# Performance work log

Measured on AMD Instinct MI355X. Metric: run time of the kernel, lower is better.

The kernel has to match this reference:

```python
import jax, jax.numpy as jnp
import numpy as np

N_NODES = 50000


def gcn_layer(x, W, b, src, dst, norm):
    # x: [N, Fin] -> [N, Fout]; PyG GCNConv: x' = D^-1/2 (A+I) D^-1/2 (x W) + b
    h = x @ W
    msg = h[src] * norm[:, None]              # gather + scale per edge (incl. self loops)
    out = jax.ops.segment_sum(msg, dst, num_segments=N_NODES)
    return out + b


def setup_inputs() -> dict:
    key = jax.random.key(0)
    ks = jax.random.split(key, 12)
    F_in, F_hid, T, E = 128, 128, 10, 1600000
    features = jax.random.normal(ks[0], (N_NODES, F_in), dtype=jnp.float32)
    edges = jax.random.randint(ks[1], (2, E), 0, N_NODES, dtype=jnp.int64)
    s = 1.0 / np.sqrt(F_in)
    W0 = jax.random.uniform(ks[2], (F_in, F_hid), jnp.float32, -s, s)
    b0 = jnp.zeros((F_hid,), jnp.float32)
    W1 = jax.random.uniform(ks[3], (F_hid, F_hid), jnp.float32, -s, s)
    b1 = jnp.zeros((F_hid,), jnp.float32)
    W2 = jax.random.uniform(ks[4], (F_hid, F_hid), jnp.float32, -s, s)
    b2 = jnp.zeros((F_hid,), jnp.float32)
    Wout = jax.random.uniform(ks[5], (F_hid, T), jnp.float32, -s, s)
    bout = jax.random.uniform(ks[6], (T,), jnp.float32, -s, s)
    return {"features": features, "edges": edges, "W0": W0, "b0": b0,
            "W1": W1, "b1": b1, "W2": W2, "b2": b2, "Wout": Wout, "bout": bout}


def reference(features, edges, W0, b0, W1, b1, W2, b2, Wout, bout):
    # Add self loops once; edge structure shared across layers.
    loop = jnp.arange(N_NODES, dtype=edges.dtype)
    src = jnp.concatenate([edges[0], loop])
    dst = jnp.concatenate([edges[1], loop])
    deg = jax.ops.segment_sum(jnp.ones_like(dst, dtype=features.dtype), dst,
                              num_segments=N_NODES)
    dinv = jnp.where(deg > 0, jax.lax.rsqrt(deg), 0.0)
    norm = dinv[src] * dinv[dst]              # [E + N]

    x = gcn_layer(features, W0, b0, src, dst, norm)
    x = gcn_layer(x, W1, b1, src, dst, norm)
    x = gcn_layer(x, W2, b2, src, dst, norm)

    pooled = jnp.mean(x, axis=0)              # [F_hid]
    logits = pooled @ Wout + bout             # [T]
    return jax.nn.log_softmax(logits, axis=0).reshape(1, -1)
```

## Files before the change

kernel.cpp:

```cpp
#include <hip/hip_runtime.h>


#define FDIM 128
#define HSZ 12500
#define NBG 64
#define BSZ 98
#define NBKT 512
#define SCB 256
#define STG 6400


__global__ void __launch_bounds__(1024)
k1_count_deg(const int* __restrict__ edges, int E, int e4, int N,
             int* __restrict__ blockCnt, int* __restrict__ partial) {
  __shared__ int h[HSZ];
  __shared__ int cnt[NBKT];
  const int t = threadIdx.x;
  const int bid = blockIdx.x;
  const int g = bid >> 6, j = bid & (NBG - 1);
  const int lo = g * HSZ;
  const int hi = min(N, lo + HSZ);
  const int hs = hi - lo;
  for (int i = t; i < hs; i += 1024) h[i] = 0;
  if (t < NBKT) cnt[t] = 0;
  __syncthreads();

  const int per4 = (e4 + SCB - 1) / SCB;
  const int i0 = bid * per4;
  const int i1 = min(e4, i0 + per4);
  const int4* s4 = (const int4*)edges;
  for (int i = i0 + t; i < i1; i += 1024) {
    int4 s = s4[i];
    atomicAdd(&cnt[s.x / BSZ], 1);
    atomicAdd(&cnt[s.y / BSZ], 1);
    atomicAdd(&cnt[s.z / BSZ], 1);
    atomicAdd(&cnt[s.w / BSZ], 1);
  }
  if (bid == 0) {
    for (int e = 4 * e4 + t; e < E; e += 1024)
      atomicAdd(&cnt[edges[e] / BSZ], 1);
  }

  const int4* d4 = (const int4*)(edges + E);
  for (int i = j * 1024 + t; i < e4; i += NBG * 1024) {
    int4 d = d4[i];
    if (d.x >= lo && d.x < hi) atomicAdd(&h[d.x - lo], 1);
    if (d.y >= lo && d.y < hi) atomicAdd(&h[d.y - lo], 1);
    if (d.z >= lo && d.z < hi) atomicAdd(&h[d.z - lo], 1);
    if (d.w >= lo && d.w < hi) atomicAdd(&h[d.w - lo], 1);
  }
  if (j == 0) {
    const int* dst = edges + E;
    for (int e = 4 * e4 + t; e < E; e += 1024) {
      int d = dst[e];
      if (d >= lo && d < hi) atomicAdd(&h[d - lo], 1);
    }
  }
  __syncthreads();
  if (t < NBKT) blockCnt[bid * NBKT + t] = cnt[t];
  int* op = partial + (size_t)bid * HSZ;
  for (int i = t; i < hs; i += 1024) op[i] = h[i];
}


__global__ void __launch_bounds__(256)
k2_scatter_dinv(const int* __restrict__ edges, int E, int e4, int N,
                const int* __restrict__ blockCnt,
                const int* __restrict__ partial,
                int* __restrict__ bucket, int* __restrict__ meta,
                float* __restrict__ dinv) {
  const int bid = blockIdx.x;
  const int t = threadIdx.x;

  if (bid >= SCB) {
    int n = (bid - SCB) * 256 + t;
    if (n < N) {
      int gg = n / HSZ, off = n - gg * HSZ;
      const int* p = partial + ((size_t)gg * NBG) * HSZ + off;
      int s = 1;
      for (int jj = 0; jj < NBG; ++jj) s += p[(size_t)jj * HSZ];
      dinv[n] = rsqrtf((float)s);
    }
    return;
  }

  __shared__ int baseS[NBKT];
  __shared__ int off2[NBKT];
  __shared__ int offRun[NBKT];
  __shared__ int cntS[NBKT];
  __shared__ int wsum[4];
  __shared__ int stg[STG];

  const int lane = t & 63, wv = t >> 6;
  const int k0 = 2 * t, k1 = 2 * t + 1;
  const int c0 = blockCnt[bid * NBKT + k0];
  const int c1 = blockCnt[bid * NBKT + k1];
  int off0 = 0, off1 = 0, tot0 = 0, tot1 = 0;
  for (int b = 0; b < SCB; ++b) {
    int v0 = blockCnt[b * NBKT + k0];
    int v1 = blockCnt[b * NBKT + k1];
    if (b < bid) { off0 += v0; off1 += v1; }
    tot0 += v0; tot1 += v1;
  }
  int s = tot0 + tot1;
  int inc = s;
  #pragma unroll
  for (int o = 1; o < 64; o <<= 1) {
    int q = __shfl_up(inc, o, 64);
    if (lane >= o) inc += q;
  }
  if (lane == 63) wsum[wv] = inc;
  __syncthreads();
  int wb = 0;
  for (int w = 0; w < wv; ++w) wb += wsum[w];
  const int ex = wb + inc - s;
  baseS[k0] = ex + off0;
  baseS[k1] = ex + tot0 + off1;
  if (bid == 0) {
    meta[k0] = ex;            meta[k1] = ex + tot0;
    meta[NBKT + k0] = tot0;   meta[NBKT + k1] = tot1;
  }
  int s2 = c0 + c1;
  int inc2 = s2;
  #pragma unroll
  for (int o = 1; o < 64; o <<= 1) {
    int q = __shfl_up(inc2, o, 64);
    if (lane >= o) inc2 += q;
  }
  __syncthreads();
  if (lane == 63) wsum[wv] = inc2;
  __syncthreads();
  int wb2 = 0;
  for (int w = 0; w < wv; ++w) wb2 += wsum[w];
  const int ex2 = wb2 + inc2 - s2;
  off2[k0] = ex2;        off2[k1] = ex2 + c0;
  offRun[k0] = ex2;      offRun[k1] = ex2 + c0;
  cntS[k0] = c0;         cntS[k1] = c1;
  __syncthreads();

  const int per4 = (e4 + SCB - 1) / SCB;
  const int i0 = bid * per4;
  const int i1 = min(e4, i0 + per4);
  const int4* s4 = (const int4*)edges;
  const int4* d4 = (const int4*)(edges + E);
  for (int i = i0 + t; i < i1; i += 256) {
    int4 sv = s4[i];
    int4 dv = d4[i];
    int b, p;
    b = sv.x / BSZ; p = atomicAdd(&offRun[b], 1); stg[p] = ((sv.x - b * BSZ) << 16) | dv.x;
    b = sv.y / BSZ; p = atomicAdd(&offRun[b], 1); stg[p] = ((sv.y - b * BSZ) << 16) | dv.y;
    b = sv.z / BSZ; p = atomicAdd(&offRun[b], 1); stg[p] = ((sv.z - b * BSZ) << 16) | dv.z;
    b = sv.w / BSZ; p = atomicAdd(&offRun[b], 1); stg[p] = ((sv.w - b * BSZ) << 16) | dv.w;
  }
  if (bid == 0) {
    for (int e = 4 * e4 + t; e < E; e += 256) {
      int sv = edges[e], dv = edges[E + e];
      int b = sv / BSZ;
      int p = atomicAdd(&offRun[b], 1);
      stg[p] = ((sv - b * BSZ) << 16) | dv;
    }
  }
  __syncthreads();
  for (int k = t; k < NBKT; k += 256) {
    const int len = cntS[k];
    const int lb = off2[k];
    const int gb = baseS[k];
    for (int i = 0; i < len; ++i)
      bucket[gb + i] = stg[lb + i];
  }
}


__global__ void __launch_bounds__(1024)
pass_kernel(const int* __restrict__ bucket, const int* __restrict__ meta,
            const float* __restrict__ dinv, const float* __restrict__ win,
            float* __restrict__ wout, float* __restrict__ ssump,
            const float* __restrict__ feat, float* __restrict__ v0p,
            int N, int doV0) {
  __shared__ float uacc[16][100];
  __shared__ float ul[BSZ];
  __shared__ float red[16];
  __shared__ float partS[8][FDIM];
  const int t = threadIdx.x;
  const int wv = t >> 6;
  const int b = blockIdx.x;
  const int n0 = b * BSZ;
  const int ns = min(BSZ, N - n0);

  for (int i = t; i < 16 * 100; i += 1024)
    ((float*)uacc)[i] = 0.f;
  __syncthreads();

  const int base = meta[b];
  const int end = base + meta[NBKT + b];
  for (int i = base + t; i < end; i += 1024) {
    int p = bucket[i];
    atomicAdd(&uacc[wv][p >> 16], win[p & 0xFFFF]);
  }
  __syncthreads();

  float u = 0.f;
  if (t < ns) {
    float s = 0.f;
    #pragma unroll
    for (int k = 0; k < 16; ++k) s += uacc[k][t];
    int n = n0 + t;
    u = dinv[n] * (s + win[n]);
    if (wout) wout[n] = dinv[n] * u;
    ul[t] = u;
  } else if (t < BSZ) {
    ul[t] = 0.f;
  }
  if (ssump) {
    float a = u;
    for (int o = 32; o > 0; o >>= 1) a += __shfl_down(a, o, 64);
    if ((t & 63) == 0) red[wv] = a;
    __syncthreads();
    if (t == 0) {
      float s = 0.f;
      #pragma unroll
      for (int k = 0; k < 16; ++k) s += red[k];
      ssump[b] = s;
    }
  }
  if (doV0) {
    __syncthreads();
    const int f = t & (FDIM - 1);
    const int r8 = t >> 7;
    float acc = 0.f;
    for (int r = r8; r < ns; r += 8)
      acc += ul[r] * feat[(size_t)(n0 + r) * FDIM + f];
    partS[r8][f] = acc;
    __syncthreads();
    if (r8 == 0) {
      float s = 0.f;
      #pragma unroll
      for (int k = 0; k < 8; ++k) s += partS[k][f];
      v0p[(size_t)b * FDIM + f] = s;
    }
  }
}


__global__ void __launch_bounds__(1024)
final_kernel(const float* __restrict__ W0, const float* __restrict__ b0,
             const float* __restrict__ W1, const float* __restrict__ b1,
             const float* __restrict__ W2, const float* __restrict__ b2,
             const float* __restrict__ Wout, const float* __restrict__ bout,
             const float* __restrict__ v0p, int nv0,
             const float* __restrict__ ssumpA,
             const float* __restrict__ ssumpB,
             int nss,
             float* __restrict__ out, int N) {
  __shared__ float Wl[FDIM * FDIM];
  __shared__ float WoL[FDIM * 10];
  __shared__ float va[FDIM], vb[FDIM];
  __shared__ float part[8][FDIM];
  __shared__ float red0[16], red1[16];
  __shared__ float shS1, shS2;
  __shared__ float lg[10];
  const int t = threadIdx.x;
  const int f = t & (FDIM - 1);
  const int sl = t >> 7;

  {
    const float4* w4 = (const float4*)W0;
    float4* l4 = (float4*)Wl;
    #pragma unroll
    for (int i = 0; i < 4; ++i) l4[t + i * 1024] = w4[t + i * 1024];
    if (t < (FDIM * 10) / 4) ((float4*)WoL)[t] = ((const float4*)Wout)[t];
  }
  float acc = 0.f;
  for (int j = sl; j < nv0; j += 8) acc += v0p[(size_t)j * FDIM + f];
  part[sl][f] = acc;
  {
    float a0 = 0.f, a1 = 0.f;
    for (int j = t; j < nss; j += 1024) { a0 += ssumpA[j]; a1 += ssumpB[j]; }
    for (int o = 32; o > 0; o >>= 1) {
      a0 += __shfl_down(a0, o, 64);
      a1 += __shfl_down(a1, o, 64);
    }
    if ((t & 63) == 0) { red0[t >> 6] = a0; red1[t >> 6] = a1; }
  }
  __syncthreads();
  if (sl == 0) {
    float s = 0.f;
    #pragma unroll
    for (int j = 0; j < 8; ++j) s += part[j][f];
    va[f] = s;
  }
  if (t == 0) {
    float x = 0.f, y = 0.f;
    #pragma unroll
    for (int i = 0; i < 16; ++i) { x += red0[i]; y += red1[i]; }
    shS2 = x; shS1 = y;
  }
  __syncthreads();

  acc = 0.f;
  #pragma unroll
  for (int k = 0; k < 16; ++k) {
    int kk = sl * 16 + k;
    acc += va[kk] * Wl[kk * FDIM + f];
  }
  part[sl][f] = acc;
  __syncthreads();
  {
    const float4* w4 = (const float4*)W1;
    float4* l4 = (float4*)Wl;
    #pragma unroll
    for (int i = 0; i < 4; ++i) l4[t + i * 1024] = w4[t + i * 1024];
  }
  if (sl == 0) {
    float s = 0.f;
    #pragma unroll
    for (int j = 0; j < 8; ++j) s += part[j][f];
    vb[f] = s + shS1 * b0[f];
  }
  __syncthreads();

  acc = 0.f;
  #pragma unroll
  for (int k = 0; k < 16; ++k) {
    int kk = sl * 16 + k;
    acc += vb[kk] * Wl[kk * FDIM + f];
  }
  part[sl][f] = acc;
  __syncthreads();
  {
    const float4* w4 = (const float4*)W2;
    float4* l4 = (float4*)Wl;
    #pragma unroll
    for (int i = 0; i < 4; ++i) l4[t + i * 1024] = w4[t + i * 1024];
  }
  if (sl == 0) {
    float s = 0.f;
    #pragma unroll
    for (int j = 0; j < 8; ++j) s += part[j][f];
    va[f] = s + shS2 * b1[f];
  }
  __syncthreads();

  acc = 0.f;
  #pragma unroll
  for (int k = 0; k < 16; ++k) {
    int kk = sl * 16 + k;
    acc += va[kk] * Wl[kk * FDIM + f];
  }
  part[sl][f] = acc;
  __syncthreads();
  if (sl == 0) {
    float s = 0.f;
    #pragma unroll
    for (int j = 0; j < 8; ++j) s += part[j][f];
    vb[f] = s / (float)N + b2[f];
  }
  __syncthreads();

  if (t < 10) {
    float a = 0.f;
    for (int k = 0; k < FDIM; ++k) a += vb[k] * WoL[k * 10 + t];
    lg[t] = a + bout[t];
  }
  __syncthreads();
  if (t == 0) {
    float m = lg[0];
    for (int q = 1; q < 10; ++q) m = fmaxf(m, lg[q]);
    float s = 0.f;
    for (int q = 0; q < 10; ++q) s += expf(lg[q] - m);
    float lse = logf(s);
    for (int q = 0; q < 10; ++q) out[q] = lg[q] - m - lse;
  }
}


__global__ void __launch_bounds__(1024)
hist_deg_kernel(const int* __restrict__ edges, int E, int e4, int N,
                int* __restrict__ partial) {
  __shared__ int h[HSZ];
  const int g = blockIdx.x / NBG;
  const int j = blockIdx.x - g * NBG;
  const int lo = g * HSZ;
  const int hi = min(N, lo + HSZ);
  const int hs = hi - lo;
  for (int i = threadIdx.x; i < hs; i += blockDim.x) h[i] = 0;
  __syncthreads();
  const int* dst = edges + E;
  const int4* dst4 = (const int4*)dst;
  for (int i = j * blockDim.x + threadIdx.x; i < e4; i += NBG * blockDim.x) {
    int4 d = dst4[i];
    if (d.x >= lo && d.x < hi) atomicAdd(&h[d.x - lo], 1);
    if (d.y >= lo && d.y < hi) atomicAdd(&h[d.y - lo], 1);
    if (d.z >= lo && d.z < hi) atomicAdd(&h[d.z - lo], 1);
    if (d.w >= lo && d.w < hi) atomicAdd(&h[d.w - lo], 1);
  }
  if (j == 0) {
    for (int e = 4 * e4 + threadIdx.x; e < E; e += blockDim.x) {
      int d = dst[e];
      if (d >= lo && d < hi) atomicAdd(&h[d - lo], 1);
    }
  }
  __syncthreads();
  int* out = partial + (size_t)blockIdx.x * HSZ;
  for (int i = threadIdx.x; i < hs; i += blockDim.x) out[i] = h[i];
}

__global__ void merge_dinv_kernel(const int* __restrict__ partial,
                                  float* __restrict__ dinv, int N) {
  int n = blockIdx.x * blockDim.x + threadIdx.x;
  if (n >= N) return;
  int g = n / HSZ;
  int off = n - g * HSZ;
  const int* p = partial + ((size_t)g * NBG) * HSZ + off;
  int s = 1;
  for (int jj = 0; jj < NBG; ++jj) s += p[(size_t)jj * HSZ];
  dinv[n] = rsqrtf((float)s);
}

__global__ void __launch_bounds__(1024)
hist_u_kernel(const int* __restrict__ edges, int E, int e4, int N,
              const float* __restrict__ w,
              float* __restrict__ partial) {
  __shared__ float h[HSZ];
  const int g = blockIdx.x / NBG;
  const int j = blockIdx.x - g * NBG;
  const int lo = g * HSZ;
  const int hi = min(N, lo + HSZ);
  const int hs = hi - lo;
  for (int i = threadIdx.x; i < hs; i += blockDim.x) h[i] = 0.f;
  __syncthreads();
  const int4* s4 = (const int4*)edges;
  const int4* d4 = (const int4*)(edges + E);
  for (int i = j * blockDim.x + threadIdx.x; i < e4; i += NBG * blockDim.x) {
    int4 s = s4[i];
    int4 d = d4[i];
    if (s.x >= lo && s.x < hi) atomicAdd(&h[s.x - lo], w[d.x]);
    if (s.y >= lo && s.y < hi) atomicAdd(&h[s.y - lo], w[d.y]);
    if (s.z >= lo && s.z < hi) atomicAdd(&h[s.z - lo], w[d.z]);
    if (s.w >= lo && s.w < hi) atomicAdd(&h[s.w - lo], w[d.w]);
  }
  if (j == 0) {
    const int* se = edges; const int* de = edges + E;
    for (int e = 4 * e4 + threadIdx.x; e < E; e += blockDim.x) {
      int s = se[e], d = de[e];
      if (s >= lo && s < hi) atomicAdd(&h[s - lo], w[d]);
    }
  }
  __syncthreads();
  float* out = partial + (size_t)blockIdx.x * HSZ;
  for (int i = threadIdx.x; i < hs; i += blockDim.x) out[i] = h[i];
}

__global__ void __launch_bounds__(256)
merge_u_kernel(const float* __restrict__ partial,
               const float* __restrict__ dinv,
               const float* __restrict__ win,
               float* __restrict__ uout,
               float* __restrict__ wout,
               float* __restrict__ ssump, int N) {
  __shared__ float red[4];
  int n = blockIdx.x * blockDim.x + threadIdx.x;
  float u = 0.f;
  if (n < N) {
    int g = n / HSZ;
    int off = n - g * HSZ;
    const float* p = partial + ((size_t)g * NBG) * HSZ + off;
    float s = 0.f;
    for (int jj = 0; jj < NBG; ++jj) s += p[(size_t)jj * HSZ];
    u = dinv[n] * (s + win[n]);
    if (uout) uout[n] = u;
    if (wout) wout[n] = dinv[n] * u;
  }
  if (ssump) {
    float a = u;
    for (int o = 32; o > 0; o >>= 1) a += __shfl_down(a, o, 64);
    if ((threadIdx.x & 63) == 0) red[threadIdx.x >> 6] = a;
    __syncthreads();
    if (threadIdx.x == 0)
      ssump[blockIdx.x] = red[0] + red[1] + red[2] + red[3];
  }
}

__global__ void __launch_bounds__(1024)
v0_kernel(const float* __restrict__ feat, const float* __restrict__ u0,
          float* __restrict__ v0p, int N) {
  __shared__ float sh[8][FDIM];
  int f = threadIdx.x & (FDIM - 1);
  int r8 = threadIdx.x >> 7;
  float acc = 0.f;
  for (int r = blockIdx.x * 8 + r8; r < N; r += 128 * 8)
    acc += u0[r] * feat[(size_t)r * FDIM + f];
  sh[r8][f] = acc;
  __syncthreads();
  if (r8 == 0) {
    float s = acc;
    #pragma unroll
    for (int k = 1; k < 8; ++k) s += sh[k][f];
    v0p[(size_t)blockIdx.x * FDIM + f] = s;
  }
}


extern "C" void kernel_launch(void* const* d_in, const int* in_sizes, int n_in,
                              void* d_out, int out_size, void* d_ws, size_t ws_size,
                              hipStream_t stream) {
  const float* feat = (const float*)d_in[0];
  const int*   edges = (const int*)d_in[1];
  const float* W0 = (const float*)d_in[2];
  const float* b0 = (const float*)d_in[3];
  const float* W1 = (const float*)d_in[4];
  const float* b1 = (const float*)d_in[5];
  const float* W2 = (const float*)d_in[6];
  const float* b2 = (const float*)d_in[7];
  const float* Wout = (const float*)d_in[8];
  const float* bout = (const float*)d_in[9];

  const int N = in_sizes[0] / FDIM;
  const int E = in_sizes[1] / 2;
  const int e4 = E >> 2;
  const int mergeGrid = (N + 255) / 256;

  char* ws = (char*)d_ws;
  size_t nb = ((size_t)N * 4 + 511) & ~(size_t)511;
  size_t partB = ((size_t)4 * NBG * HSZ * 4 + 511) & ~(size_t)511;
  size_t v0pB = ((size_t)NBKT * FDIM * 4 + 511) & ~(size_t)511;
  size_t ssBsz = ((size_t)NBKT * 4 + 511) & ~(size_t)511;
  size_t bktB = ((size_t)E * 4 + 511) & ~(size_t)511;
  size_t cntB = (size_t)SCB * NBKT * 4;
  size_t need = partB + 4 * nb + v0pB + 2 * ssBsz + bktB + cntB + 8192;

  char* p = ws;
  float* part = (float*)p;       p += partB;
  float* dinv = (float*)p;       p += nb;
  float* w2   = (float*)p;       p += nb;
  float* w1   = (float*)p;       p += nb;
  float* u0   = (float*)p;       p += nb;
  float* v0p  = (float*)p;       p += v0pB;
  float* ssA  = (float*)p;       p += ssBsz;
  float* ssB_ = (float*)p;       p += ssBsz;
  int* bucket = (int*)p;         p += bktB;
  int* blockCnt = (int*)p;       p += cntB;
  int* meta   = (int*)p;

  const int perBlkEdges = ((e4 + SCB - 1) / SCB) * 4 + 4;
  const bool bucketOK = (ws_size >= need) && (N <= NBKT * BSZ) &&
                        (N <= 65535) && (perBlkEdges <= STG) && ((E & 3) == 0);

  if (bucketOK) {
    k1_count_deg<<<SCB, 1024, 0, stream>>>(edges, E, e4, N,
                                           blockCnt, (int*)part);
    k2_scatter_dinv<<<SCB + mergeGrid, 256, 0, stream>>>(
        edges, E, e4, N, blockCnt, (const int*)part, bucket, meta, dinv);
    pass_kernel<<<NBKT, 1024, 0, stream>>>(bucket, meta, dinv, dinv,
                                           w2, ssA, nullptr, nullptr, N, 0);
    pass_kernel<<<NBKT, 1024, 0, stream>>>(bucket, meta, dinv, w2,
                                           w1, ssB_, nullptr, nullptr, N, 0);
    pass_kernel<<<NBKT, 1024, 0, stream>>>(bucket, meta, dinv, w1,
                                           nullptr, nullptr, feat, v0p, N, 1);
    final_kernel<<<1, 1024, 0, stream>>>(W0, b0, W1, b1, W2, b2, Wout, bout,
                                         v0p, NBKT, ssA, ssB_, NBKT,
                                         (float*)d_out, N);
  } else {
    hist_deg_kernel<<<4 * NBG, 1024, 0, stream>>>(edges, E, e4, N, (int*)part);
    merge_dinv_kernel<<<mergeGrid, 256, 0, stream>>>((const int*)part, dinv, N);
    hist_u_kernel<<<4 * NBG, 1024, 0, stream>>>(edges, E, e4, N, dinv, part);
    merge_u_kernel<<<mergeGrid, 256, 0, stream>>>(part, dinv, dinv,
                                                  nullptr, w2, ssA, N);
    hist_u_kernel<<<4 * NBG, 1024, 0, stream>>>(edges, E, e4, N, w2, part);
    merge_u_kernel<<<mergeGrid, 256, 0, stream>>>(part, dinv, w2,
                                                  nullptr, w1, ssB_, N);
    hist_u_kernel<<<4 * NBG, 1024, 0, stream>>>(edges, E, e4, N, w1, part);
    merge_u_kernel<<<mergeGrid, 256, 0, stream>>>(part, dinv, w1,
                                                  u0, nullptr, nullptr, N);
    v0_kernel<<<128, 1024, 0, stream>>>(feat, u0, v0p, N);
    final_kernel<<<1, 1024, 0, stream>>>(W0, b0, W1, b1, W2, b2, Wout, bout,
                                         v0p, 128, ssA, ssB_, mergeGrid,
                                         (float*)d_out, N);
  }
}
```

Before: 103.6 us.

## Pack degree histogram into 16-bit counters, parallelize bucket copy, drop weight staging

The degree histogram now packs two 16-bit counters into each 32-bit shared word. Each block covers twice as many nodes, so 128 blocks per group each scan half as many edges, and the merge kernel reads half as many partial words, emitting two dinv values per word. The bucket copy-out in the scatter kernel now uses 16 lanes per bucket instead of one thread walking each bucket serially, giving coalesced writes. The final kernel reads W0/W1/W2 directly from global memory instead of staging them in 64KB of shared memory. The risk is 16-bit overflow if any per-block partial degree exceeds 65535.

```diff
diff --git a/kernel.cpp b/kernel.cpp
--- a/kernel.cpp
+++ b/kernel.cpp
@@ -2,6 +2,8 @@
 
 
 #define FDIM 128
+#define DHSZ 25000
+#define DNB 128
 #define HSZ 12500
 #define NBG 64
 #define BSZ 98
@@ -12,16 +14,17 @@
 
 __global__ void __launch_bounds__(1024)
 k1_count_deg(const int* __restrict__ edges, int E, int e4, int N,
-             int* __restrict__ blockCnt, int* __restrict__ partial) {
-  __shared__ int h[HSZ];
+             int* __restrict__ blockCnt, unsigned int* __restrict__ partial) {
+  __shared__ unsigned int h32[DHSZ / 2];
   __shared__ int cnt[NBKT];
   const int t = threadIdx.x;
   const int bid = blockIdx.x;
-  const int g = bid >> 6, j = bid & (NBG - 1);
-  const int lo = g * HSZ;
-  const int hi = min(N, lo + HSZ);
-  const int hs = hi - lo;
-  for (int i = t; i < hs; i += 1024) h[i] = 0;
+  const int g = bid >> 7, j = bid & (DNB - 1);
+  const int lo = g * DHSZ;
+  const int hi = min(N, lo + DHSZ);
+  const int hs = max(0, hi - lo);
+  const int hw = (hs + 1) >> 1;
+  for (int i = t; i < hw; i += 1024) h32[i] = 0u;
   if (t < NBKT) cnt[t] = 0;
   __syncthreads();
 
@@ -42,45 +45,48 @@
   }
 
   const int4* d4 = (const int4*)(edges + E);
-  for (int i = j * 1024 + t; i < e4; i += NBG * 1024) {
+  for (int i = j * 1024 + t; i < e4; i += DNB * 1024) {
     int4 d = d4[i];
-    if (d.x >= lo && d.x < hi) atomicAdd(&h[d.x - lo], 1);
-    if (d.y >= lo && d.y < hi) atomicAdd(&h[d.y - lo], 1);
-    if (d.z >= lo && d.z < hi) atomicAdd(&h[d.z - lo], 1);
-    if (d.w >= lo && d.w < hi) atomicAdd(&h[d.w - lo], 1);
+    if (d.x >= lo && d.x < hi) { int l = d.x - lo; atomicAdd(&h32[l >> 1], 1u << ((l & 1) << 4)); }
+    if (d.y >= lo && d.y < hi) { int l = d.y - lo; atomicAdd(&h32[l >> 1], 1u << ((l & 1) << 4)); }
+    if (d.z >= lo && d.z < hi) { int l = d.z - lo; atomicAdd(&h32[l >> 1], 1u << ((l & 1) << 4)); }
+    if (d.w >= lo && d.w < hi) { int l = d.w - lo; atomicAdd(&h32[l >> 1], 1u << ((l & 1) << 4)); }
   }
   if (j == 0) {
     const int* dst = edges + E;
     for (int e = 4 * e4 + t; e < E; e += 1024) {
       int d = dst[e];
-      if (d >= lo && d < hi) atomicAdd(&h[d - lo], 1);
+      if (d >= lo && d < hi) { int l = d - lo; atomicAdd(&h32[l >> 1], 1u << ((l & 1) << 4)); }
     }
   }
   __syncthreads();
   if (t < NBKT) blockCnt[bid * NBKT + t] = cnt[t];
-  int* op = partial + (size_t)bid * HSZ;
-  for (int i = t; i < hs; i += 1024) op[i] = h[i];
+  unsigned int* op = partial + (size_t)bid * (DHSZ / 2);
+  for (int i = t; i < hw; i += 1024) op[i] = h32[i];
 }
 
 
 __global__ void __launch_bounds__(256)
 k2_scatter_dinv(const int* __restrict__ edges, int E, int e4, int N,
                 const int* __restrict__ blockCnt,
-                const int* __restrict__ partial,
+                const unsigned int* __restrict__ partial,
                 int* __restrict__ bucket, int* __restrict__ meta,
                 float* __restrict__ dinv) {
   const int bid = blockIdx.x;
   const int t = threadIdx.x;
 
   if (bid >= SCB) {
-    int n = (bid - SCB) * 256 + t;
-    if (n < N) {
-      int gg = n / HSZ, off = n - gg * HSZ;
-      const int* p = partial + ((size_t)gg * NBG) * HSZ + off;
-      int s = 1;
-      for (int jj = 0; jj < NBG; ++jj) s += p[(size_t)jj * HSZ];
-      dinv[n] = rsqrtf((float)s);
-    }
+    int q = (bid - SCB) * 256 + t;
+    if (q >= 2 * (DHSZ / 2)) return;
+    int g = q / (DHSZ / 2);
+    int word = q - g * (DHSZ / 2);
+    int n0 = g * DHSZ + 2 * word;
+    if (n0 >= N) return;
+    const unsigned int* p = partial + ((size_t)g * DNB) * (DHSZ / 2) + word;
+    unsigned int sum = 0;
+    for (int jj = 0; jj < DNB; ++jj) sum += p[(size_t)jj * (DHSZ / 2)];
+    dinv[n0] = rsqrtf((float)((sum & 0xFFFFu) + 1u));
+    if (n0 + 1 < N) dinv[n0 + 1] = rsqrtf((float)((sum >> 16) + 1u));
     return;
   }
 
@@ -161,11 +167,12 @@
     }
   }
   __syncthreads();
-  for (int k = t; k < NBKT; k += 256) {
+  const int sub = t >> 4, ln16 = t & 15;
+  for (int k = sub; k < NBKT; k += 16) {
     const int len = cntS[k];
     const int lb = off2[k];
     const int gb = baseS[k];
-    for (int i = 0; i < len; ++i)
+    for (int i = ln16; i < len; i += 16)
       bucket[gb + i] = stg[lb + i];
   }
 }
@@ -252,7 +259,6 @@
              const float* __restrict__ ssumpB,
              int nss,
              float* __restrict__ out, int N) {
-  __shared__ float Wl[FDIM * FDIM];
   __shared__ float WoL[FDIM * 10];
   __shared__ float va[FDIM], vb[FDIM];
   __shared__ float part[8][FDIM];
@@ -263,13 +269,7 @@
   const int f = t & (FDIM - 1);
   const int sl = t >> 7;
 
-  {
-    const float4* w4 = (const float4*)W0;
-    float4* l4 = (float4*)Wl;
-    #pragma unroll
-    for (int i = 0; i < 4; ++i) l4[t + i * 1024] = w4[t + i * 1024];
-    if (t < (FDIM * 10) / 4) ((float4*)WoL)[t] = ((const float4*)Wout)[t];
-  }
+  if (t < (FDIM * 10) / 4) ((float4*)WoL)[t] = ((const float4*)Wout)[t];
   float acc = 0.f;
   for (int j = sl; j < nv0; j += 8) acc += v0p[(size_t)j * FDIM + f];
   part[sl][f] = acc;
@@ -301,16 +301,10 @@
   #pragma unroll
   for (int k = 0; k < 16; ++k) {
     int kk = sl * 16 + k;
-    acc += va[kk] * Wl[kk * FDIM + f];
+    acc += va[kk] * W0[kk * FDIM + f];
   }
   part[sl][f] = acc;
   __syncthreads();
-  {
-    const float4* w4 = (const float4*)W1;
-    float4* l4 = (float4*)Wl;
-    #pragma unroll
-    for (int i = 0; i < 4; ++i) l4[t + i * 1024] = w4[t + i * 1024];
-  }
   if (sl == 0) {
     float s = 0.f;
     #pragma unroll
@@ -323,16 +317,10 @@
   #pragma unroll
   for (int k = 0; k < 16; ++k) {
     int kk = sl * 16 + k;
-    acc += vb[kk] * Wl[kk * FDIM + f];
+    acc += vb[kk] * W1[kk * FDIM + f];
   }
   part[sl][f] = acc;
   __syncthreads();
-  {
-    const float4* w4 = (const float4*)W2;
-    float4* l4 = (float4*)Wl;
-    #pragma unroll
-    for (int i = 0; i < 4; ++i) l4[t + i * 1024] = w4[t + i * 1024];
-  }
   if (sl == 0) {
     float s = 0.f;
     #pragma unroll
@@ -345,7 +333,7 @@
   #pragma unroll
   for (int k = 0; k < 16; ++k) {
     int kk = sl * 16 + k;
-    acc += va[kk] * Wl[kk * FDIM + f];
+    acc += va[kk] * W2[kk * FDIM + f];
   }
   part[sl][f] = acc;
   __syncthreads();
@@ -544,13 +532,16 @@
 
   const int perBlkEdges = ((e4 + SCB - 1) / SCB) * 4 + 4;
   const bool bucketOK = (ws_size >= need) && (N <= NBKT * BSZ) &&
-                        (N <= 65535) && (perBlkEdges <= STG) && ((E & 3) == 0);
+                        (N <= 2 * DHSZ) && (N <= 65535) &&
+                        (perBlkEdges <= STG) && ((E & 3) == 0);
 
   if (bucketOK) {
+    const int dinvBlocks = (2 * (DHSZ / 2) + 255) / 256;
     k1_count_deg<<<SCB, 1024, 0, stream>>>(edges, E, e4, N,
-                                           blockCnt, (int*)part);
-    k2_scatter_dinv<<<SCB + mergeGrid, 256, 0, stream>>>(
-        edges, E, e4, N, blockCnt, (const int*)part, bucket, meta, dinv);
+                                           blockCnt, (unsigned int*)part);
+    k2_scatter_dinv<<<SCB + dinvBlocks, 256, 0, stream>>>(
+        edges, E, e4, N, blockCnt, (const unsigned int*)part,
+        bucket, meta, dinv);
     pass_kernel<<<NBKT, 1024, 0, stream>>>(bucket, meta, dinv, dinv,
                                            w2, ssA, nullptr, nullptr, N, 0);
     pass_kernel<<<NBKT, 1024, 0, stream>>>(bucket, meta, dinv, w2,
```

After: 105.5 us. No clear change (+1.8%).
